# Kernel optimization log

Measured on AMD Instinct MI355X. Metric: run time of the kernel, lower is better.

Reference implementation:

```python
import jax, jax.numpy as jnp
import numpy as np

N_NODES, N_EDGES, N_GRAPHS = 50000, 800000, 512
F_IN, HID, DIM_OUT = 128, 256, 16


def setup_inputs() -> dict:
    key = jax.random.key(0)
    ks = jax.random.split(key, 16)
    glorot = lambda k, fi, fo: jax.random.normal(k, (fi, fo), jnp.float32) * jnp.sqrt(2.0 / (fi + fo))
    return {
        "x": jax.random.normal(ks[0], (N_NODES, F_IN), jnp.float32),
        "edge_index": jax.random.randint(ks[1], (2, N_EDGES), 0, N_NODES, dtype=jnp.int32),
        "batch": jnp.sort(jax.random.randint(ks[2], (N_NODES,), 0, N_GRAPHS, dtype=jnp.int32)),
        "mol_wt": jax.random.uniform(ks[3], (N_GRAPHS, 1), jnp.float32),
        "n_rings": jax.random.uniform(ks[4], (N_GRAPHS, 1), jnp.float32),
        "W1": glorot(ks[5], F_IN, HID), "b1": jnp.zeros((HID,), jnp.float32),
        "W2": glorot(ks[6], HID, HID), "b2": jnp.zeros((HID,), jnp.float32),
        "W3": glorot(ks[7], HID, HID), "b3": jnp.zeros((HID,), jnp.float32),
        "fcW1": glorot(ks[8], HID + 2, 196), "fcb1": jnp.zeros((196,), jnp.float32),
        "fcW2": glorot(ks[9], 196, DIM_OUT), "fcb2": jnp.zeros((DIM_OUT,), jnp.float32),
    }


def _gcn_conv(x, W, b, src, dst, deg_inv_sqrt, n_nodes):
    # PyG GCNConv: linear transform, then D^-1/2 (A+I) D^-1/2 aggregation, then bias
    xw = x @ W  # [N, HID]
    norm = deg_inv_sqrt[src] * deg_inv_sqrt[dst]  # [E+N]
    msg = norm[:, None] * xw[src]  # gather + scale
    out = jax.ops.segment_sum(msg, dst, num_segments=n_nodes)  # scatter-add at targets
    return out + b


def reference(x, edge_index, batch, mol_wt, n_rings,
              W1, b1, W2, b2, W3, b3, fcW1, fcb1, fcW2, fcb2):
    n_nodes = x.shape[0]
    self_loop = jnp.arange(n_nodes, dtype=edge_index.dtype)
    src = jnp.concatenate([edge_index[0], self_loop])
    dst = jnp.concatenate([edge_index[1], self_loop])
    deg = jax.ops.segment_sum(jnp.ones_like(dst, dtype=x.dtype), dst, num_segments=n_nodes)
    deg_inv_sqrt = jnp.where(deg > 0, jax.lax.rsqrt(deg), 0.0)

    h = jax.nn.relu(_gcn_conv(x, W1, b1, src, dst, deg_inv_sqrt, n_nodes))
    h = jax.nn.relu(_gcn_conv(h, W2, b2, src, dst, deg_inv_sqrt, n_nodes))
    h = jax.nn.relu(_gcn_conv(h, W3, b3, src, dst, deg_inv_sqrt, n_nodes))

    n_graphs = mol_wt.shape[0]
    sums = jax.ops.segment_sum(h, batch, num_segments=n_graphs)
    counts = jax.ops.segment_sum(jnp.ones((n_nodes,), h.dtype), batch, num_segments=n_graphs)
    hg = sums / jnp.maximum(counts, 1.0)[:, None]  # global mean pool

    hg = jnp.concatenate([hg, mol_wt, n_rings], axis=1)  # [G, 258]
    hg = jax.nn.relu(hg @ fcW1 + fcb1)
    return hg @ fcW2 + fcb2
```

## Files before the change

### kernel.cpp

```cpp
#include <hip/hip_runtime.h>

#define NN 50000
#define NE 800000
#define NG 512
#define FIN 128
#define HID 256
#define NBUK 196

typedef short short8 __attribute__((ext_vector_type(8)));
typedef float f32x4 __attribute__((ext_vector_type(4)));

static inline int cdiv(int a, int b) { return (a + b - 1) / b; }

static __device__ inline unsigned short f2bf(float f) {
    unsigned int u = __float_as_uint(f);
    unsigned int r = (u + 0x7FFF + ((u >> 16) & 1)) >> 16;
    return (unsigned short)r;
}
static __device__ inline float bf2f(unsigned short h) {
    return __uint_as_float(((unsigned int)h) << 16);
}
static __device__ inline float bflo(unsigned int p) { return __uint_as_float(p << 16); }
static __device__ inline float bfhi(unsigned int p) { return __uint_as_float(p & 0xFFFF0000u); }

typedef __attribute__((address_space(1))) unsigned int gu32;
typedef __attribute__((address_space(3))) unsigned int lu32;
static __device__ __forceinline__ void gload16(const unsigned short* g, unsigned short* l) {
    __builtin_amdgcn_global_load_lds((const gu32*)(const void*)g, (lu32*)(void*)l, 16, 0, 0);
}


__global__ __launch_bounds__(256) void hist_bucket_kernel(const int* __restrict__ dst,
                                                          int* __restrict__ gbuk) {
    __shared__ int lh[NBUK];
    int tid = threadIdx.x;
    for (int j = tid; j < NBUK; j += 256) lh[j] = 0;
    __syncthreads();
    int base = blockIdx.x * 2048;
    #pragma unroll
    for (int k = 0; k < 8; ++k) {
        int i = base + k * 256 + tid;
        if (i < NE) atomicAdd(&lh[dst[i] >> 8], 1);
    }
    __syncthreads();
    for (int j = tid; j < NBUK; j += 256) if (lh[j]) atomicAdd(&gbuk[j], lh[j]);
}

__global__ void goff_bukscan_kernel(const int* __restrict__ batch, int* __restrict__ goff,
                                    const int* __restrict__ gbuk, int* __restrict__ bukoff,
                                    int* __restrict__ bukcur) {
    if (blockIdx.x < 196) {
        int i = blockIdx.x * 256 + threadIdx.x;
        if (i >= NN) return;
        int b = batch[i];
        int pb = (i == 0) ? -1 : batch[i - 1];
        for (int g = pb + 1; g <= b; ++g) goff[g] = i;
        if (i == NN - 1) for (int g = b + 1; g <= NG; ++g) goff[g] = NN;
    } else {
        __shared__ int ws[4];
        int tid = threadIdx.x, lane = tid & 63, wid = tid >> 6;
        int v = (tid < NBUK) ? gbuk[tid] : 0;
        int incl = v;
        #pragma unroll
        for (int off = 1; off < 64; off <<= 1) {
            int u = __shfl_up(incl, off, 64);
            if (lane >= off) incl += u;
        }
        if (lane == 63) ws[wid] = incl;
        __syncthreads();
        int woff = 0;
        for (int w = 0; w < wid; ++w) woff += ws[w];
        int ex = woff + incl - v;
        if (tid < NBUK) { bukoff[tid] = ex; bukcur[tid] = ex; }
        if (tid == NBUK - 1) bukoff[NBUK] = ex + v;
    }
}

__global__ __launch_bounds__(256) void scatter_kernel(const int* __restrict__ src,
                                                      const int* __restrict__ dst,
                                                      int* __restrict__ bukcur,
                                                      unsigned int* __restrict__ pairs) {
    __shared__ int lh[NBUK];
    __shared__ int lbase[NBUK];
    int tid = threadIdx.x;
    for (int j = tid; j < NBUK; j += 256) lh[j] = 0;
    __syncthreads();
    int base = blockIdx.x * 2048;
    int d[8], s[8];
    #pragma unroll
    for (int k = 0; k < 8; ++k) {
        int i = base + k * 256 + tid;
        if (i < NE) {
            d[k] = dst[i]; s[k] = src[i];
            atomicAdd(&lh[d[k] >> 8], 1);
        } else d[k] = -1;
    }
    __syncthreads();
    for (int j = tid; j < NBUK; j += 256) lbase[j] = lh[j] ? atomicAdd(&bukcur[j], lh[j]) : 0;
    __syncthreads();
    for (int j = tid; j < NBUK; j += 256) lh[j] = 0;
    __syncthreads();
    #pragma unroll
    for (int k = 0; k < 8; ++k) {
        if (d[k] >= 0) {
            int b = d[k] >> 8;
            int loc = atomicAdd(&lh[b], 1);
            pairs[lbase[b] + loc] = ((unsigned int)s[k] << 16) | (unsigned int)(d[k] & 255);
        }
    }
}

__global__ __launch_bounds__(256) void local_csr_kernel(const unsigned int* __restrict__ pairs,
                                                        const int* __restrict__ bukoff,
                                                        int* __restrict__ row_ptr,
                                                        int* __restrict__ col,
                                                        float* __restrict__ dis) {
    __shared__ int fcnt[256];
    __shared__ int foff[256];
    __shared__ int fws[4];
    int b = blockIdx.x, tid = threadIdx.x;
    int beg = bukoff[b], end = bukoff[b + 1];
    fcnt[tid] = 0;
    __syncthreads();
    for (int i = beg + tid; i < end; i += 256) atomicAdd(&fcnt[pairs[i] & 255], 1);
    __syncthreads();
    int lane = tid & 63, wid = tid >> 6;
    int v = fcnt[tid], incl = v;
    #pragma unroll
    for (int off = 1; off < 64; off <<= 1) {
        int u = __shfl_up(incl, off, 64);
        if (lane >= off) incl += u;
    }
    if (lane == 63) fws[wid] = incl;
    __syncthreads();
    int woff = 0;
    for (int w = 0; w < wid; ++w) woff += fws[w];
    int ex = woff + incl - v;
    foff[tid] = ex;
    int gid = b * 256 + tid;
    if (gid < NN) {
        row_ptr[gid] = beg + ex;
        dis[gid] = rsqrtf((float)v + 1.0f);
    }
    if (b == 0 && tid == 0) row_ptr[NN] = NE;
    __syncthreads();
    for (int i = beg + tid; i < end; i += 256) {
        unsigned int p = pairs[i];
        int loc = atomicAdd(&foff[p & 255], 1);
        col[beg + loc] = (int)(p >> 16);
    }
}

#define CAST1 (NN * FIN / 4)
__global__ void castall_kernel(const float* __restrict__ x, const float* __restrict__ dis,
                               unsigned short* __restrict__ Xs,
                               const float* __restrict__ W1, const float* __restrict__ W2,
                               const float* __restrict__ W3,
                               unsigned short* __restrict__ W1t, unsigned short* __restrict__ W2t,
                               unsigned short* __restrict__ W3t) {
    int idx = blockIdx.x * 256 + threadIdx.x;
    if (idx < CAST1) {
        float dv = dis[idx >> 5];
        float4 v = ((const float4*)x)[idx];
        ushort4 o;
        o.x = f2bf(dv * v.x); o.y = f2bf(dv * v.y); o.z = f2bf(dv * v.z); o.w = f2bf(dv * v.w);
        ((ushort4*)Xs)[idx] = o;
        return;
    }
    int t = idx - CAST1;
    if (t < FIN * 256) {
        int n = t / FIN, k = t - n * FIN;
        W1t[t] = f2bf(W1[(size_t)k * 256 + n]);
    } else if (t < FIN * 256 + HID * 256) {
        int t2 = t - FIN * 256;
        int n = t2 / HID, k = t2 - n * HID;
        W2t[t2] = f2bf(W2[(size_t)k * 256 + n]);
    } else if (t < FIN * 256 + 2 * HID * 256) {
        int t3 = t - FIN * 256 - HID * 256;
        int n = t3 / HID, k = t3 - n * HID;
        W3t[t3] = f2bf(W3[(size_t)k * 256 + n]);
    }
}

template <int MODE>
__global__ __launch_bounds__(256) void gemm128_kernel(
        const unsigned short* __restrict__ A, const unsigned short* __restrict__ Bt,
        const float* __restrict__ dis, const float* __restrict__ bias,
        unsigned short* __restrict__ Cout, int M, int K) {
    __shared__ unsigned short As[2][128 * 32];
    __shared__ unsigned short Bs[2][128 * 32];
    const int tid = threadIdx.x;
    const int bm = blockIdx.x * 128, bn = blockIdx.y * 128;
    const int wave = tid >> 6, lane = tid & 63;
    const int l16 = lane & 15, quad = lane >> 4;
    const int wm = (wave & 1) * 64, wn = (wave >> 1) * 64;

    const int srow0 = tid >> 2, skc = (tid & 3) * 8;
    const int srow1 = (256 + tid) >> 2;
    int ar0 = bm + srow0; if (ar0 > M - 1) ar0 = M - 1;
    int ar1 = bm + srow1; if (ar1 > M - 1) ar1 = M - 1;
    const unsigned short* a0 = A + (size_t)ar0 * K + skc;
    const unsigned short* a1 = A + (size_t)ar1 * K + skc;
    const unsigned short* b0 = Bt + (size_t)(bn + srow0) * K + skc;
    const unsigned short* b1 = Bt + (size_t)(bn + srow1) * K + skc;

    f32x4 acc[4][4];
    #pragma unroll
    for (int i = 0; i < 4; ++i)
        #pragma unroll
        for (int j = 0; j < 4; ++j) acc[i][j] = (f32x4){0.f, 0.f, 0.f, 0.f};

    gload16(a0, &As[0][(size_t)tid * 8]);
    gload16(a1, &As[0][(size_t)(256 + tid) * 8]);
    gload16(b0, &Bs[0][(size_t)tid * 8]);
    gload16(b1, &Bs[0][(size_t)(256 + tid) * 8]);

    int cur = 0;
    for (int k0 = 0; k0 < K; k0 += 32) {
        __syncthreads();
        int nxt = cur ^ 1;
        if (k0 + 32 < K) {
            gload16(a0 + k0 + 32, &As[nxt][(size_t)tid * 8]);
            gload16(a1 + k0 + 32, &As[nxt][(size_t)(256 + tid) * 8]);
            gload16(b0 + k0 + 32, &Bs[nxt][(size_t)tid * 8]);
            gload16(b1 + k0 + 32, &Bs[nxt][(size_t)(256 + tid) * 8]);
        }
        short8 af[4], bf[4];
        #pragma unroll
        for (int mt = 0; mt < 4; ++mt) af[mt] = *(const short8*)&As[cur][(wm + mt * 16 + l16) * 32 + quad * 8];
        #pragma unroll
        for (int nt = 0; nt < 4; ++nt) bf[nt] = *(const short8*)&Bs[cur][(wn + nt * 16 + l16) * 32 + quad * 8];
        #pragma unroll
        for (int mt = 0; mt < 4; ++mt)
            #pragma unroll
            for (int nt = 0; nt < 4; ++nt)
                acc[mt][nt] = __builtin_amdgcn_mfma_f32_16x16x32_bf16(af[mt], bf[nt], acc[mt][nt], 0, 0, 0);
        cur = nxt;
    }
    float bv[4];
    #pragma unroll
    for (int nt = 0; nt < 4; ++nt) bv[nt] = bias[bn + wn + nt * 16 + l16];
    #pragma unroll
    for (int mt = 0; mt < 4; ++mt) {
        #pragma unroll
        for (int r = 0; r < 4; ++r) {
            int row = bm + wm + mt * 16 + quad * 4 + r;
            if (row < M) {
                unsigned short* crow = Cout + (size_t)row * HID + bn + wn + l16;
                if (MODE == 0) {
                    float dv = dis[row];
                    #pragma unroll
                    for (int nt = 0; nt < 4; ++nt)
                        crow[nt * 16] = f2bf(dv * fmaxf(acc[mt][nt][r] + bv[nt], 0.f));
                } else {
                    #pragma unroll
                    for (int nt = 0; nt < 4; ++nt)
                        crow[nt * 16] = f2bf(fmaxf(acc[mt][nt][r] + bv[nt], 0.f));
                }
            }
        }
    }
}

__global__ __launch_bounds__(256) void agg128_kernel(
        const unsigned short* __restrict__ Xs, const int* __restrict__ row_ptr,
        const int* __restrict__ col, const float* __restrict__ dis,
        unsigned short* __restrict__ Xa, int n) {
    int node = blockIdx.x * 4 + (threadIdx.x >> 6);
    if (node >= n) return;
    int lane = threadIdx.x & 63;
    const unsigned int* Xv = (const unsigned int*)Xs;
    unsigned int p = Xv[(size_t)node * 64 + lane];
    float ax = bflo(p), ay = bfhi(p);
    int e = row_ptr[node], end = row_ptr[node + 1];
    for (; e + 7 < end; e += 8) {
        unsigned int m[8];
        #pragma unroll
        for (int j = 0; j < 8; ++j) m[j] = Xv[(size_t)col[e + j] * 64 + lane];
        #pragma unroll
        for (int j = 0; j < 8; ++j) { ax += bflo(m[j]); ay += bfhi(m[j]); }
    }
    for (; e < end; ++e) {
        unsigned int m = Xv[(size_t)col[e] * 64 + lane];
        ax += bflo(m); ay += bfhi(m);
    }
    float dv = dis[node];
    unsigned int o = (unsigned int)f2bf(dv * ax) | ((unsigned int)f2bf(dv * ay) << 16);
    ((unsigned int*)Xa)[(size_t)node * 64 + lane] = o;
}

__global__ __launch_bounds__(256) void agg256_kernel(
        const unsigned short* __restrict__ Hs, const int* __restrict__ row_ptr,
        const int* __restrict__ col, const float* __restrict__ dis,
        unsigned short* __restrict__ G, int n) {
    int node = blockIdx.x * 4 + (threadIdx.x >> 6);
    if (node >= n) return;
    int lane = threadIdx.x & 63;
    const uint2* Hv = (const uint2*)Hs;
    uint2 p = Hv[(size_t)node * 64 + lane];
    float4 acc = make_float4(bflo(p.x), bfhi(p.x), bflo(p.y), bfhi(p.y));
    int e = row_ptr[node], end = row_ptr[node + 1];
    for (; e + 7 < end; e += 8) {
        uint2 m[8];
        #pragma unroll
        for (int j = 0; j < 8; ++j) m[j] = Hv[(size_t)col[e + j] * 64 + lane];
        #pragma unroll
        for (int j = 0; j < 8; ++j) {
            acc.x += bflo(m[j].x); acc.y += bfhi(m[j].x);
            acc.z += bflo(m[j].y); acc.w += bfhi(m[j].y);
        }
    }
    for (; e < end; ++e) {
        uint2 m = Hv[(size_t)col[e] * 64 + lane];
        acc.x += bflo(m.x); acc.y += bfhi(m.x);
        acc.z += bflo(m.y); acc.w += bfhi(m.y);
    }
    float dv = dis[node];
    ushort4 o;
    o.x = f2bf(dv * acc.x); o.y = f2bf(dv * acc.y);
    o.z = f2bf(dv * acc.z); o.w = f2bf(dv * acc.w);
    ((ushort4*)G)[(size_t)node * 64 + lane] = o;
}

__global__ __launch_bounds__(256) void pool_mlp_kernel(
        const unsigned short* __restrict__ H, const int* __restrict__ goff,
        const float* __restrict__ mol, const float* __restrict__ rings,
        const float* __restrict__ fcW1, const float* __restrict__ fcb1,
        const float* __restrict__ fcW2, const float* __restrict__ fcb2,
        float* __restrict__ out) {
    __shared__ float s_hg[258];
    __shared__ float s_t[196];
    int g = blockIdx.x, tid = threadIdx.x;
    int beg = goff[g], end = goff[g + 1];
    float acc = 0.f;
    for (int i = beg; i < end; ++i) acc += bf2f(H[(size_t)i * HID + tid]);
    s_hg[tid] = acc / fmaxf((float)(end - beg), 1.0f);
    if (tid == 0) { s_hg[256] = mol[g]; s_hg[257] = rings[g]; }
    __syncthreads();
    if (tid < 196) {
        float a = fcb1[tid];
        for (int k = 0; k < 258; ++k) a = fmaf(s_hg[k], fcW1[k * 196 + tid], a);
        s_t[tid] = fmaxf(a, 0.f);
    }
    __syncthreads();
    if (tid < 16) {
        float a = fcb2[tid];
        for (int k = 0; k < 196; ++k) a = fmaf(s_t[k], fcW2[k * 16 + tid], a);
        out[g * 16 + tid] = a;
    }
}

extern "C" void kernel_launch(void* const* d_in, const int* in_sizes, int n_in,
                              void* d_out, int out_size, void* d_ws, size_t ws_size,
                              hipStream_t stream) {
    const float* x     = (const float*)d_in[0];
    const int*   ei    = (const int*)d_in[1];
    const int*   batch = (const int*)d_in[2];
    const float* mol   = (const float*)d_in[3];
    const float* rings = (const float*)d_in[4];
    const float* W1 = (const float*)d_in[5];
    const float* b1 = (const float*)d_in[6];
    const float* W2 = (const float*)d_in[7];
    const float* b2 = (const float*)d_in[8];
    const float* W3 = (const float*)d_in[9];
    const float* b3 = (const float*)d_in[10];
    const float* fcW1 = (const float*)d_in[11];
    const float* fcb1 = (const float*)d_in[12];
    const float* fcW2 = (const float*)d_in[13];
    const float* fcb2 = (const float*)d_in[14];
    float* out = (float*)d_out;
    const int* src = ei;
    const int* dst = ei + NE;

    char* w = (char*)d_ws;
    auto alloc = [&](size_t bytes) {
        char* p = w;
        w += (bytes + 255) & ~(size_t)255;
        return p;
    };
    int*   gbuk    = (int*)alloc((size_t)NBUK * 4);
    int*   bukoff  = (int*)alloc((size_t)(NBUK + 1) * 4);
    int*   bukcur  = (int*)alloc((size_t)NBUK * 4);
    int*   row_ptr = (int*)alloc((size_t)(NN + 1) * 4);
    int*   goff    = (int*)alloc((size_t)(NG + 1) * 4);
    float* dis     = (float*)alloc((size_t)NN * 4);
    unsigned int* pairs = (unsigned int*)alloc((size_t)NE * 4);
    int*   col     = (int*)alloc((size_t)NE * 4);
    unsigned short* Xs  = (unsigned short*)alloc((size_t)NN * FIN * 2);
    unsigned short* Xa  = (unsigned short*)alloc((size_t)NN * FIN * 2);
    unsigned short* Hs  = (unsigned short*)alloc((size_t)NN * HID * 2);
    unsigned short* Ga  = (unsigned short*)alloc((size_t)NN * HID * 2);
    unsigned short* Hf  = (unsigned short*)alloc((size_t)NN * HID * 2);
    unsigned short* W1t = (unsigned short*)alloc((size_t)FIN * HID * 2);
    unsigned short* W2t = (unsigned short*)alloc((size_t)HID * HID * 2);
    unsigned short* W3t = (unsigned short*)alloc((size_t)HID * HID * 2);

    hipMemsetAsync(gbuk, 0, (size_t)NBUK * 4, stream);
    int eb = cdiv(NE, 2048);
    hist_bucket_kernel<<<eb, 256, 0, stream>>>(dst, gbuk);
    goff_bukscan_kernel<<<197, 256, 0, stream>>>(batch, goff, gbuk, bukoff, bukcur);
    scatter_kernel<<<eb, 256, 0, stream>>>(src, dst, bukcur, pairs);
    local_csr_kernel<<<NBUK, 256, 0, stream>>>(pairs, bukoff, row_ptr, col, dis);

    int ctotal = CAST1 + (FIN + 2 * HID) * 256;
    castall_kernel<<<cdiv(ctotal, 256), 256, 0, stream>>>(x, dis, Xs, W1, W2, W3, W1t, W2t, W3t);

    dim3 ggrid(cdiv(NN, 128), 2);
    int agrid = cdiv(NN, 4);
    agg128_kernel<<<agrid, 256, 0, stream>>>(Xs, row_ptr, col, dis, Xa, NN);
    gemm128_kernel<0><<<ggrid, 256, 0, stream>>>(Xa, W1t, dis, b1, Hs, NN, FIN);
    agg256_kernel<<<agrid, 256, 0, stream>>>(Hs, row_ptr, col, dis, Ga, NN);
    gemm128_kernel<0><<<ggrid, 256, 0, stream>>>(Ga, W2t, dis, b2, Hs, NN, HID);
    agg256_kernel<<<agrid, 256, 0, stream>>>(Hs, row_ptr, col, dis, Ga, NN);
    gemm128_kernel<1><<<ggrid, 256, 0, stream>>>(Ga, W3t, dis, b3, Hf, NN, HID);
    pool_mlp_kernel<<<NG, 256, 0, stream>>>(Hf, goff, mol, rings, fcW1, fcb1, fcW2, fcb2, out);
}
```

Before: 408.7 us.

## Fuse neighbor aggregation into GEMM with 64-row tiles held in shared memory

```diff
diff --git a/kernel.cpp b/kernel.cpp
--- a/kernel.cpp
+++ b/kernel.cpp
@@ -182,144 +182,111 @@
     }
 }
 
-template <int MODE>
-__global__ __launch_bounds__(256) void gemm128_kernel(
-        const unsigned short* __restrict__ A, const unsigned short* __restrict__ Bt,
-        const float* __restrict__ dis, const float* __restrict__ bias,
-        unsigned short* __restrict__ Cout, int M, int K) {
-    __shared__ unsigned short As[2][128 * 32];
-    __shared__ unsigned short Bs[2][128 * 32];
+template <int KD, int MODE>
+__global__ __launch_bounds__(256) void fused_agg_gemm_kernel(
+        const unsigned short* __restrict__ Src, const int* __restrict__ row_ptr,
+        const int* __restrict__ col, const float* __restrict__ dis,
+        const unsigned short* __restrict__ Bt, const float* __restrict__ bias,
+        unsigned short* __restrict__ Cout) {
+    constexpr int LDA = (KD == 128) ? 130 : 258;
+    __shared__ unsigned short As[64 * LDA];
+    __shared__ unsigned short Bs[256 * 32];
     const int tid = threadIdx.x;
-    const int bm = blockIdx.x * 128, bn = blockIdx.y * 128;
     const int wave = tid >> 6, lane = tid & 63;
     const int l16 = lane & 15, quad = lane >> 4;
-    const int wm = (wave & 1) * 64, wn = (wave >> 1) * 64;
-
-    const int srow0 = tid >> 2, skc = (tid & 3) * 8;
-    const int srow1 = (256 + tid) >> 2;
-    int ar0 = bm + srow0; if (ar0 > M - 1) ar0 = M - 1;
-    int ar1 = bm + srow1; if (ar1 > M - 1) ar1 = M - 1;
-    const unsigned short* a0 = A + (size_t)ar0 * K + skc;
-    const unsigned short* a1 = A + (size_t)ar1 * K + skc;
-    const unsigned short* b0 = Bt + (size_t)(bn + srow0) * K + skc;
-    const unsigned short* b1 = Bt + (size_t)(bn + srow1) * K + skc;
-
-    f32x4 acc[4][4];
-    #pragma unroll
-    for (int i = 0; i < 4; ++i)
+    const int bm = blockIdx.x * 64;
+
+    for (int i = 0; i < 16; ++i) {
+        int lrow = wave * 16 + i;
+        int node = bm + lrow;
+        if (KD == 128) {
+            unsigned int o = 0;
+            if (node < NN) {
+                const unsigned int* Xv = (const unsigned int*)Src;
+                unsigned int p = Xv[(size_t)node * 64 + lane];
+                float ax = bflo(p), ay = bfhi(p);
+                int e = row_ptr[node], end = row_ptr[node + 1];
+                for (; e + 7 < end; e += 8) {
+                    unsigned int m[8];
+                    #pragma unroll
+                    for (int j = 0; j < 8; ++j) m[j] = Xv[(size_t)col[e + j] * 64 + lane];
+                    #pragma unroll
+                    for (int j = 0; j < 8; ++j) { ax += bflo(m[j]); ay += bfhi(m[j]); }
+                }
+                for (; e < end; ++e) {
+                    unsigned int m = Xv[(size_t)col[e] * 64 + lane];
+                    ax += bflo(m); ay += bfhi(m);
+                }
+                float dv = dis[node];
+                o = (unsigned int)f2bf(dv * ax) | ((unsigned int)f2bf(dv * ay) << 16);
+            }
+            *(unsigned int*)&As[lrow * LDA + lane * 2] = o;
+        } else {
+            uint2 o = make_uint2(0, 0);
+            if (node < NN) {
+                const uint2* Hv = (const uint2*)Src;
+                uint2 p = Hv[(size_t)node * 64 + lane];
+                float4 acc = make_float4(bflo(p.x), bfhi(p.x), bflo(p.y), bfhi(p.y));
+                int e = row_ptr[node], end = row_ptr[node + 1];
+                for (; e + 7 < end; e += 8) {
+                    uint2 m[8];
+                    #pragma unroll
+                    for (int j = 0; j < 8; ++j) m[j] = Hv[(size_t)col[e + j] * 64 + lane];
+                    #pragma unroll
+                    for (int j = 0; j < 8; ++j) {
+                        acc.x += bflo(m[j].x); acc.y += bfhi(m[j].x);
+                        acc.z += bflo(m[j].y); acc.w += bfhi(m[j].y);
+                    }
+                }
+                for (; e < end; ++e) {
+                    uint2 m = Hv[(size_t)col[e] * 64 + lane];
+                    acc.x += bflo(m.x); acc.y += bfhi(m.x);
+                    acc.z += bflo(m.y); acc.w += bfhi(m.y);
+                }
+                float dv = dis[node];
+                o.x = (unsigned int)f2bf(dv * acc.x) | ((unsigned int)f2bf(dv * acc.y) << 16);
+                o.y = (unsigned int)f2bf(dv * acc.z) | ((unsigned int)f2bf(dv * acc.w) << 16);
+            }
+            *(uint2*)&As[lrow * LDA + lane * 4] = o;
+        }
+    }
+    __syncthreads();
+
+    f32x4 acc[16];
+    #pragma unroll
+    for (int i = 0; i < 16; ++i) acc[i] = (f32x4){0.f, 0.f, 0.f, 0.f};
+
+    const int brow = tid >> 2, bkc = (tid & 3) * 8;
+    for (int k0 = 0; k0 < KD; k0 += 32) {
         #pragma unroll
-        for (int j = 0; j < 4; ++j) acc[i][j] = (f32x4){0.f, 0.f, 0.f, 0.f};
-
-    gload16(a0, &As[0][(size_t)tid * 8]);
-    gload16(a1, &As[0][(size_t)(256 + tid) * 8]);
-    gload16(b0, &Bs[0][(size_t)tid * 8]);
-    gload16(b1, &Bs[0][(size_t)(256 + tid) * 8]);
-
-    int cur = 0;
-    for (int k0 = 0; k0 < K; k0 += 32) {
+        for (int j = 0; j < 4; ++j)
+            gload16(Bt + (size_t)(j * 64 + brow) * KD + k0 + bkc, &Bs[(size_t)(j * 256 + tid) * 8]);
         __syncthreads();
-        int nxt = cur ^ 1;
-        if (k0 + 32 < K) {
-            gload16(a0 + k0 + 32, &As[nxt][(size_t)tid * 8]);
-            gload16(a1 + k0 + 32, &As[nxt][(size_t)(256 + tid) * 8]);
-            gload16(b0 + k0 + 32, &Bs[nxt][(size_t)tid * 8]);
-            gload16(b1 + k0 + 32, &Bs[nxt][(size_t)(256 + tid) * 8]);
-        }
-        short8 af[4], bf[4];
+        short8 af = *(const short8*)&As[(wave * 16 + l16) * LDA + k0 + quad * 8];
         #pragma unroll
-        for (int mt = 0; mt < 4; ++mt) af[mt] = *(const short8*)&As[cur][(wm + mt * 16 + l16) * 32 + quad * 8];
-        #pragma unroll
-        for (int nt = 0; nt < 4; ++nt) bf[nt] = *(const short8*)&Bs[cur][(wn + nt * 16 + l16) * 32 + quad * 8];
-        #pragma unroll
-        for (int mt = 0; mt < 4; ++mt)
+        for (int nt = 0; nt < 16; ++nt) {
+            short8 bf = *(const short8*)&Bs[(nt * 16 + l16) * 32 + quad * 8];
+            acc[nt] = __builtin_amdgcn_mfma_f32_16x16x32_bf16(af, bf, acc[nt], 0, 0, 0);
+        }
+        __syncthreads();
+    }
+    float bv[16];
+    #pragma unroll
+    for (int nt = 0; nt < 16; ++nt) bv[nt] = bias[nt * 16 + l16];
+    #pragma unroll
+    for (int r = 0; r < 4; ++r) {
+        int grow = bm + wave * 16 + quad * 4 + r;
+        if (grow < NN) {
+            unsigned short* crow = Cout + (size_t)grow * HID + l16;
+            float dv = (MODE == 0) ? dis[grow] : 1.0f;
             #pragma unroll
-            for (int nt = 0; nt < 4; ++nt)
-                acc[mt][nt] = __builtin_amdgcn_mfma_f32_16x16x32_bf16(af[mt], bf[nt], acc[mt][nt], 0, 0, 0);
-        cur = nxt;
-    }
-    float bv[4];
-    #pragma unroll
-    for (int nt = 0; nt < 4; ++nt) bv[nt] = bias[bn + wn + nt * 16 + l16];
-    #pragma unroll
-    for (int mt = 0; mt < 4; ++mt) {
-        #pragma unroll
-        for (int r = 0; r < 4; ++r) {
-            int row = bm + wm + mt * 16 + quad * 4 + r;
-            if (row < M) {
-                unsigned short* crow = Cout + (size_t)row * HID + bn + wn + l16;
-                if (MODE == 0) {
-                    float dv = dis[row];
-                    #pragma unroll
-                    for (int nt = 0; nt < 4; ++nt)
-                        crow[nt * 16] = f2bf(dv * fmaxf(acc[mt][nt][r] + bv[nt], 0.f));
-                } else {
-                    #pragma unroll
-                    for (int nt = 0; nt < 4; ++nt)
-                        crow[nt * 16] = f2bf(fmaxf(acc[mt][nt][r] + bv[nt], 0.f));
-                }
+            for (int nt = 0; nt < 16; ++nt) {
+                float v = fmaxf(acc[nt][r] + bv[nt], 0.f);
+                if (MODE == 0) v *= dv;
+                crow[nt * 16] = f2bf(v);
             }
         }
     }
-}
-
-__global__ __launch_bounds__(256) void agg128_kernel(
-        const unsigned short* __restrict__ Xs, const int* __restrict__ row_ptr,
-        const int* __restrict__ col, const float* __restrict__ dis,
-        unsigned short* __restrict__ Xa, int n) {
-    int node = blockIdx.x * 4 + (threadIdx.x >> 6);
-    if (node >= n) return;
-    int lane = threadIdx.x & 63;
-    const unsigned int* Xv = (const unsigned int*)Xs;
-    unsigned int p = Xv[(size_t)node * 64 + lane];
-    float ax = bflo(p), ay = bfhi(p);
-    int e = row_ptr[node], end = row_ptr[node + 1];
-    for (; e + 7 < end; e += 8) {
-        unsigned int m[8];
-        #pragma unroll
-        for (int j = 0; j < 8; ++j) m[j] = Xv[(size_t)col[e + j] * 64 + lane];
-        #pragma unroll
-        for (int j = 0; j < 8; ++j) { ax += bflo(m[j]); ay += bfhi(m[j]); }
-    }
-    for (; e < end; ++e) {
-        unsigned int m = Xv[(size_t)col[e] * 64 + lane];
-        ax += bflo(m); ay += bfhi(m);
-    }
-    float dv = dis[node];
-    unsigned int o = (unsigned int)f2bf(dv * ax) | ((unsigned int)f2bf(dv * ay) << 16);
-    ((unsigned int*)Xa)[(size_t)node * 64 + lane] = o;
-}
-
-__global__ __launch_bounds__(256) void agg256_kernel(
-        const unsigned short* __restrict__ Hs, const int* __restrict__ row_ptr,
-        const int* __restrict__ col, const float* __restrict__ dis,
-        unsigned short* __restrict__ G, int n) {
-    int node = blockIdx.x * 4 + (threadIdx.x >> 6);
-    if (node >= n) return;
-    int lane = threadIdx.x & 63;
-    const uint2* Hv = (const uint2*)Hs;
-    uint2 p = Hv[(size_t)node * 64 + lane];
-    float4 acc = make_float4(bflo(p.x), bfhi(p.x), bflo(p.y), bfhi(p.y));
-    int e = row_ptr[node], end = row_ptr[node + 1];
-    for (; e + 7 < end; e += 8) {
-        uint2 m[8];
-        #pragma unroll
-        for (int j = 0; j < 8; ++j) m[j] = Hv[(size_t)col[e + j] * 64 + lane];
-        #pragma unroll
-        for (int j = 0; j < 8; ++j) {
-            acc.x += bflo(m[j].x); acc.y += bfhi(m[j].x);
-            acc.z += bflo(m[j].y); acc.w += bfhi(m[j].y);
-        }
-    }
-    for (; e < end; ++e) {
-        uint2 m = Hv[(size_t)col[e] * 64 + lane];
-        acc.x += bflo(m.x); acc.y += bfhi(m.x);
-        acc.z += bflo(m.y); acc.w += bfhi(m.y);
-    }
-    float dv = dis[node];
-    ushort4 o;
-    o.x = f2bf(dv * acc.x); o.y = f2bf(dv * acc.y);
-    o.z = f2bf(dv * acc.z); o.w = f2bf(dv * acc.w);
-    ((ushort4*)G)[(size_t)node * 64 + lane] = o;
 }
 
 __global__ __launch_bounds__(256) void pool_mlp_kernel(
@@ -387,9 +354,8 @@
     unsigned int* pairs = (unsigned int*)alloc((size_t)NE * 4);
     int*   col     = (int*)alloc((size_t)NE * 4);
     unsigned short* Xs  = (unsigned short*)alloc((size_t)NN * FIN * 2);
-    unsigned short* Xa  = (unsigned short*)alloc((size_t)NN * FIN * 2);
     unsigned short* Hs  = (unsigned short*)alloc((size_t)NN * HID * 2);
-    unsigned short* Ga  = (unsigned short*)alloc((size_t)NN * HID * 2);
+    unsigned short* Hs2 = (unsigned short*)alloc((size_t)NN * HID * 2);
     unsigned short* Hf  = (unsigned short*)alloc((size_t)NN * HID * 2);
     unsigned short* W1t = (unsigned short*)alloc((size_t)FIN * HID * 2);
     unsigned short* W2t = (unsigned short*)alloc((size_t)HID * HID * 2);
@@ -405,13 +371,9 @@
     int ctotal = CAST1 + (FIN + 2 * HID) * 256;
     castall_kernel<<<cdiv(ctotal, 256), 256, 0, stream>>>(x, dis, Xs, W1, W2, W3, W1t, W2t, W3t);
 
-    dim3 ggrid(cdiv(NN, 128), 2);
-    int agrid = cdiv(NN, 4);
-    agg128_kernel<<<agrid, 256, 0, stream>>>(Xs, row_ptr, col, dis, Xa, NN);
-    gemm128_kernel<0><<<ggrid, 256, 0, stream>>>(Xa, W1t, dis, b1, Hs, NN, FIN);
-    agg256_kernel<<<agrid, 256, 0, stream>>>(Hs, row_ptr, col, dis, Ga, NN);
-    gemm128_kernel<0><<<ggrid, 256, 0, stream>>>(Ga, W2t, dis, b2, Hs, NN, HID);
-    agg256_kernel<<<agrid, 256, 0, stream>>>(Hs, row_ptr, col, dis, Ga, NN);
-    gemm128_kernel<1><<<ggrid, 256, 0, stream>>>(Ga, W3t, dis, b3, Hf, NN, HID);
+    const int fgrid = cdiv(NN, 64);
+    fused_agg_gemm_kernel<128, 0><<<fgrid, 256, 0, stream>>>(Xs, row_ptr, col, dis, W1t, b1, Hs);
+    fused_agg_gemm_kernel<256, 0><<<fgrid, 256, 0, stream>>>(Hs, row_ptr, col, dis, W2t, b2, Hs2);
+    fused_agg_gemm_kernel<256, 1><<<fgrid, 256, 0, stream>>>(Hs2, row_ptr, col, dis, W3t, b3, Hf);
     pool_mlp_kernel<<<NG, 256, 0, stream>>>(Hf, goff, mol, rings, fcW1, fcb1, fcW2, fcb2, out);
 }
```

Measured after the change: 600.7 us. 47.0% more time.

## Load 64-wide K chunks per barrier in GEMM and split aggregation launches

Applied to the files above, without the earlier changes.

```diff
diff --git a/kernel.cpp b/kernel.cpp
--- a/kernel.cpp
+++ b/kernel.cpp
@@ -210,32 +210,30 @@
         #pragma unroll
         for (int j = 0; j < 4; ++j) acc[i][j] = (f32x4){0.f, 0.f, 0.f, 0.f};
 
-    gload16(a0, &As[0][(size_t)tid * 8]);
-    gload16(a1, &As[0][(size_t)(256 + tid) * 8]);
-    gload16(b0, &Bs[0][(size_t)tid * 8]);
-    gload16(b1, &Bs[0][(size_t)(256 + tid) * 8]);
-
-    int cur = 0;
-    for (int k0 = 0; k0 < K; k0 += 32) {
+    for (int k0 = 0; k0 < K; k0 += 64) {
+        gload16(a0 + k0,      &As[0][(size_t)tid * 8]);
+        gload16(a1 + k0,      &As[0][(size_t)(256 + tid) * 8]);
+        gload16(a0 + k0 + 32, &As[1][(size_t)tid * 8]);
+        gload16(a1 + k0 + 32, &As[1][(size_t)(256 + tid) * 8]);
+        gload16(b0 + k0,      &Bs[0][(size_t)tid * 8]);
+        gload16(b1 + k0,      &Bs[0][(size_t)(256 + tid) * 8]);
+        gload16(b0 + k0 + 32, &Bs[1][(size_t)tid * 8]);
+        gload16(b1 + k0 + 32, &Bs[1][(size_t)(256 + tid) * 8]);
         __syncthreads();
-        int nxt = cur ^ 1;
-        if (k0 + 32 < K) {
-            gload16(a0 + k0 + 32, &As[nxt][(size_t)tid * 8]);
-            gload16(a1 + k0 + 32, &As[nxt][(size_t)(256 + tid) * 8]);
-            gload16(b0 + k0 + 32, &Bs[nxt][(size_t)tid * 8]);
-            gload16(b1 + k0 + 32, &Bs[nxt][(size_t)(256 + tid) * 8]);
+        #pragma unroll
+        for (int h = 0; h < 2; ++h) {
+            short8 af[4], bf[4];
+            #pragma unroll
+            for (int mt = 0; mt < 4; ++mt) af[mt] = *(const short8*)&As[h][(wm + mt * 16 + l16) * 32 + quad * 8];
+            #pragma unroll
+            for (int nt = 0; nt < 4; ++nt) bf[nt] = *(const short8*)&Bs[h][(wn + nt * 16 + l16) * 32 + quad * 8];
+            #pragma unroll
+            for (int mt = 0; mt < 4; ++mt)
+                #pragma unroll
+                for (int nt = 0; nt < 4; ++nt)
+                    acc[mt][nt] = __builtin_amdgcn_mfma_f32_16x16x32_bf16(af[mt], bf[nt], acc[mt][nt], 0, 0, 0);
         }
-        short8 af[4], bf[4];
-        #pragma unroll
-        for (int mt = 0; mt < 4; ++mt) af[mt] = *(const short8*)&As[cur][(wm + mt * 16 + l16) * 32 + quad * 8];
-        #pragma unroll
-        for (int nt = 0; nt < 4; ++nt) bf[nt] = *(const short8*)&Bs[cur][(wn + nt * 16 + l16) * 32 + quad * 8];
-        #pragma unroll
-        for (int mt = 0; mt < 4; ++mt)
-            #pragma unroll
-            for (int nt = 0; nt < 4; ++nt)
-                acc[mt][nt] = __builtin_amdgcn_mfma_f32_16x16x32_bf16(af[mt], bf[nt], acc[mt][nt], 0, 0, 0);
-        cur = nxt;
+        __syncthreads();
     }
     float bv[4];
     #pragma unroll
@@ -292,8 +290,8 @@
 __global__ __launch_bounds__(256) void agg256_kernel(
         const unsigned short* __restrict__ Hs, const int* __restrict__ row_ptr,
         const int* __restrict__ col, const float* __restrict__ dis,
-        unsigned short* __restrict__ G, int n) {
-    int node = blockIdx.x * 4 + (threadIdx.x >> 6);
+        unsigned short* __restrict__ G, int base, int n) {
+    int node = base + blockIdx.x * 4 + (threadIdx.x >> 6);
     if (node >= n) return;
     int lane = threadIdx.x & 63;
     const uint2* Hv = (const uint2*)Hs;
@@ -407,11 +405,15 @@
 
     dim3 ggrid(cdiv(NN, 128), 2);
     int agrid = cdiv(NN, 4);
+    const int HALF = 25000;
+    int hgrid = HALF / 4;
     agg128_kernel<<<agrid, 256, 0, stream>>>(Xs, row_ptr, col, dis, Xa, NN);
     gemm128_kernel<0><<<ggrid, 256, 0, stream>>>(Xa, W1t, dis, b1, Hs, NN, FIN);
-    agg256_kernel<<<agrid, 256, 0, stream>>>(Hs, row_ptr, col, dis, Ga, NN);
+    agg256_kernel<<<hgrid, 256, 0, stream>>>(Hs, row_ptr, col, dis, Ga, 0, NN);
+    agg256_kernel<<<hgrid, 256, 0, stream>>>(Hs, row_ptr, col, dis, Ga, HALF, NN);
     gemm128_kernel<0><<<ggrid, 256, 0, stream>>>(Ga, W2t, dis, b2, Hs, NN, HID);
-    agg256_kernel<<<agrid, 256, 0, stream>>>(Hs, row_ptr, col, dis, Ga, NN);
+    agg256_kernel<<<hgrid, 256, 0, stream>>>(Hs, row_ptr, col, dis, Ga, 0, NN);
+    agg256_kernel<<<hgrid, 256, 0, stream>>>(Hs, row_ptr, col, dis, Ga, HALF, NN);
     gemm128_kernel<1><<<ggrid, 256, 0, stream>>>(Ga, W3t, dis, b3, Hf, NN, HID);
     pool_mlp_kernel<<<NG, 256, 0, stream>>>(Hf, goff, mol, rings, fcW1, fcb1, fcW2, fcb2, out);
 }
```

Result: no change. 415.9 us (+1.8%).
